# Performance work log

Hardware: AMD Instinct MI355X
Metric: run time of the kernel (lower is better)

Reference implementation:

```python
import jax, jax.numpy as jnp
import numpy as np

B, S, D, N, HD, M = 2, 2048, 1024, 16, 64, 4096  # batch, seq, d_model, heads, head_dim, d_mlp


def setup_inputs() -> dict:
    key = jax.random.key(0)
    ks = jax.random.split(key, 8)
    sd = 1.0 / np.sqrt(D)
    return {
        "x": jax.random.normal(ks[0], (B, S, D), dtype=jnp.float32),
        "W_qkv": jax.random.normal(ks[1], (N, D, 3 * HD), dtype=jnp.float32) * sd,
        "W_out": jax.random.normal(ks[2], (N, HD, D), dtype=jnp.float32) * sd,
        "ln1_w": jnp.ones((D,), jnp.float32),
        "ln1_b": jnp.zeros((D,), jnp.float32),
        "ln2_w": jnp.ones((D,), jnp.float32),
        "ln2_b": jnp.zeros((D,), jnp.float32),
        "W1": jax.random.normal(ks[3], (D, M), dtype=jnp.float32) * sd,
        "b1": jnp.zeros((M,), jnp.float32),
        "W2": jax.random.normal(ks[4], (M, D), dtype=jnp.float32) / np.sqrt(M),
        "b2": jnp.zeros((D,), jnp.float32),
    }


def _layernorm(x, w, b, eps=1e-4):
    mu = jnp.mean(x, axis=-1, keepdims=True)
    var = jnp.var(x, axis=-1, keepdims=True, ddof=1)  # torch unbiased var
    return w * (x - mu) / jnp.sqrt(var + eps) + b


def _attention(x, W_qkv, W_out):
    b, s, d = x.shape
    qkv = jnp.einsum('bsd,ndh->bnsh', x, W_qkv)  # [b,n,s,3*hd]
    q, k, v = jnp.split(qkv, 3, axis=-1)
    hd = q.shape[-1]
    attn = jnp.einsum('bnqh,bnkh->bnqk', q, k) / np.sqrt(hd)
    mask = -1e10 * (1.0 - jnp.tril(jnp.ones((s, s), jnp.float32)))
    attn = jax.nn.softmax(attn + mask, axis=-1)
    out = jnp.einsum('bnqk,bnkh->bnqh', attn, v)  # [b,n,s,hd]
    # faithful to torch: raw memory reinterpretation (b,n,s,hd) -> (b, n*hd, s)
    out = out.reshape(b, -1, s)
    # faithful to torch: d is a shared free index -> W_out summed over (n,h)
    out = jnp.einsum('bds,nhd->bsd', out, W_out)
    return out


def _mlp(x, W1, b1, W2, b2):
    h = jax.nn.gelu(x @ W1 + b1, approximate=False)
    return h @ W2 + b2


def reference(x, W_qkv, W_out, ln1_w, ln1_b, ln2_w, ln2_b, W1, b1, W2, b2):
    x = x + _attention(_layernorm(x, ln1_w, ln1_b), W_qkv, W_out)
    x = x + _mlp(_layernorm(x, ln2_w, ln2_b), W1, b1, W2, b2)
    return x
```

## Files before the change

kernel.cpp:

```cpp
#include <hip/hip_runtime.h>

typedef unsigned short ushort_t;
typedef __attribute__((ext_vector_type(8))) short short8;
typedef __attribute__((ext_vector_type(4))) float floatx4;
typedef __attribute__((ext_vector_type(4))) unsigned short ushort4v;

#define B_ 2
#define S_ 2048
#define D_ 1024
#define NH_ 16
#define HD_ 64
#define M_ 4096

#define KSCALE 0.18033688011112042f

__device__ __forceinline__ ushort_t f2bf(float f) {
    unsigned u = __builtin_bit_cast(unsigned, f);
    return (ushort_t)((u + 0x7FFFu + ((u >> 16) & 1u)) >> 16);
}

__device__ __forceinline__ void gload_lds16(const ushort_t* g, ushort_t* l) {
    __builtin_amdgcn_global_load_lds(
        (const __attribute__((address_space(1))) unsigned int*)(g),
        (__attribute__((address_space(3))) unsigned int*)(l), 16, 0, 0);
}

__device__ __forceinline__ void transpose_slab(
    const float* __restrict__ src, ushort_t* __restrict__ dst,
    int srs, int drs, int by, int bx, int tid, ushort_t* L) {
    const int tx = tid & 15, ty = tid >> 4;
    const float* s0 = src + (size_t)(by * 256 + ty * 4) * srs + bx * 64 + tx * 4;
    #pragma unroll
    for (int i = 0; i < 4; ++i) {
        float a[4][4];
        #pragma unroll
        for (int r = 0; r < 4; ++r) {
            float4 m = *(const float4*)(s0 + (size_t)(i * 64 + r) * srs);
            a[r][0] = m.x; a[r][1] = m.y; a[r][2] = m.z; a[r][3] = m.w;
        }
        const int p = i * 8 + (ty >> 1), plow = ty & 1;
        #pragma unroll
        for (int j = 0; j < 4; ++j) {
            const int c = tx * 4 + j;
            const int pp = p ^ tx;
            ushort4v t;
            t[0] = f2bf(a[0][j]); t[1] = f2bf(a[1][j]);
            t[2] = f2bf(a[2][j]); t[3] = f2bf(a[3][j]);
            *(ushort4v*)&L[c * 256 + (pp * 2 + plow) * 4] = t;
        }
    }
    __syncthreads();
    const int k = tid & 31, cg = tid >> 5;
    #pragma unroll
    for (int it = 0; it < 8; ++it) {
        const int c = it * 8 + cg;
        const int pp = k ^ (c >> 2);
        *(short8*)(dst + (size_t)(bx * 64 + c) * drs + by * 256 + k * 8) =
            *(const short8*)&L[c * 256 + pp * 8];
    }
}

__device__ __forceinline__ void ln_row_wave(const float* __restrict__ x,
                                            const float* __restrict__ w,
                                            const float* __restrict__ b,
                                            ushort_t* __restrict__ out, int row, int l) {
    const float* xr = x + (size_t)row * D_;
    float4 v[4]; float s = 0.f, ss = 0.f;
    #pragma unroll
    for (int i = 0; i < 4; ++i) {
        v[i] = *(const float4*)(xr + (i * 64 + l) * 4);
        s += v[i].x + v[i].y + v[i].z + v[i].w;
        ss += v[i].x * v[i].x + v[i].y * v[i].y + v[i].z * v[i].z + v[i].w * v[i].w;
    }
    #pragma unroll
    for (int off = 32; off >= 1; off >>= 1) { s += __shfl_xor(s, off); ss += __shfl_xor(ss, off); }
    float mu = s * (1.f / D_);
    float var = (ss - (float)D_ * mu * mu) * (1.f / (D_ - 1));
    float rstd = rsqrtf(var + 1e-4f);
    #pragma unroll
    for (int i = 0; i < 4; ++i) {
        int d = (i * 64 + l) * 4;
        float4 wv = *(const float4*)(w + d);
        float4 bv = *(const float4*)(b + d);
        ushort4v o;
        o[0] = f2bf((v[i].x - mu) * rstd * wv.x + bv.x);
        o[1] = f2bf((v[i].y - mu) * rstd * wv.y + bv.y);
        o[2] = f2bf((v[i].z - mu) * rstd * wv.z + bv.z);
        o[3] = f2bf((v[i].w - mu) * rstd * wv.w + bv.w);
        *(ushort4v*)&out[(size_t)row * D_ + d] = o;
    }
}

__global__ __launch_bounds__(256) void ln4_kernel(const float* __restrict__ x,
                                                  const float* __restrict__ w,
                                                  const float* __restrict__ b,
                                                  ushort_t* __restrict__ out) {
    ln_row_wave(x, w, b, out, blockIdx.x * 4 + (threadIdx.x >> 6), threadIdx.x & 63);
}

__global__ __launch_bounds__(256) void prep_kernel(
    const float* __restrict__ W_qkv, const float* __restrict__ W1,
    const float* __restrict__ W2, const float* __restrict__ W_out,
    ushort_t* __restrict__ WqkvT, ushort_t* __restrict__ W1T,
    ushort_t* __restrict__ W2T, float* __restrict__ wsum,
    const float* __restrict__ x, const float* __restrict__ ln1_w,
    const float* __restrict__ ln1_b, ushort_t* __restrict__ ln1_out) {
    __shared__ __align__(16) ushort_t L[64 * 256];
    const int bid = blockIdx.x;
    const int tid = threadIdx.x;
    if (bid < 192) {
        int bz = bid / 12, rem = bid % 12;
        transpose_slab(W_qkv + (size_t)bz * D_ * 192, WqkvT + (size_t)bz * 192 * D_,
                       192, D_, rem / 3, rem % 3, tid, L);
    } else if (bid < 448) {
        int r = bid - 192;
        transpose_slab(W1, W1T, M_, D_, r >> 6, r & 63, tid, L);
    } else if (bid < 704) {
        int r = bid - 448;
        transpose_slab(W2, W2T, D_, M_, r >> 4, r & 15, tid, L);
    } else if (bid < 712) {
        int cb = bid - 704;
        float4* part = (float4*)L;
        int tx = tid & 31, rg = tid >> 5;
        int col = cb * 128 + tx * 4;
        float4 s = {0.f, 0.f, 0.f, 0.f};
        for (int r = rg; r < NH_ * HD_; r += 8) {
            float4 v = *(const float4*)(W_out + (size_t)r * D_ + col);
            s.x += v.x; s.y += v.y; s.z += v.z; s.w += v.w;
        }
        part[tid] = s;
        __syncthreads();
        if (tid < 32) {
            float4 t = {0.f, 0.f, 0.f, 0.f};
            #pragma unroll
            for (int g = 0; g < 8; ++g) {
                float4 p = part[g * 32 + tid];
                t.x += p.x; t.y += p.y; t.z += p.z; t.w += p.w;
            }
            *(float4*)(wsum + cb * 128 + tid * 4) = t;
        }
    } else {
        ln_row_wave(x, ln1_w, ln1_b, ln1_out, (bid - 712) * 4 + (tid >> 6), tid & 63);
    }
}

__global__ __launch_bounds__(256) void gather_resid(
    const float* __restrict__ x, const float* __restrict__ attn,
    const float* __restrict__ wsum, float* __restrict__ x1) {
    __shared__ float tile[128][65];
    const int tid = threadIdx.x;
    const int dchunk = blockIdx.x;
    const int stile = blockIdx.y;
    const int b = stile >> 5, shi = stile & 31;
    const int h = tid & 63;
    const int wv = tid >> 6;
    #pragma unroll
    for (int r = 0; r < 32; ++r) {
        int dloc = r * 4 + wv;
        int d = dchunk * 128 + dloc;
        int q = ((d & 63) << 5) + shi;
        tile[dloc][h] = attn[((size_t)(b * NH_ + (d >> 6)) * S_ + q) * HD_ + h];
    }
    __syncthreads();
    const int row0 = b * S_ + shi * 64;
    const int dcol = tid & 127;
    const int d = dchunk * 128 + dcol;
    const float wsd = wsum[d];
    #pragma unroll
    for (int r = 0; r < 32; ++r) {
        int sr = r * 2 + (tid >> 7);
        size_t idx = (size_t)(row0 + sr) * D_ + d;
        x1[idx] = x[idx] + wsd * tile[dcol][sr];
    }
}

__global__ __launch_bounds__(256) void mlp2_reduce(
    const float* __restrict__ part, const float* __restrict__ x1,
    const float* __restrict__ b2, float* __restrict__ out) {
    int i = blockIdx.x * 256 + threadIdx.x;
    #pragma unroll
    for (int it = 0; it < 4; ++it, i += 1024 * 256) {
        size_t o = (size_t)i * 4;
        float4 s = *(const float4*)(x1 + o);
        float4 bb = *(const float4*)(b2 + ((i * 4) & (D_ - 1)));
        s.x += bb.x; s.y += bb.y; s.z += bb.z; s.w += bb.w;
        #pragma unroll
        for (int z = 0; z < 2; ++z) {
            float4 p = *(const float4*)(part + (size_t)z * ((size_t)B_ * S_ * D_) + o);
            s.x += p.x; s.y += p.y; s.z += p.z; s.w += p.w;
        }
        *(float4*)(out + o) = s;
    }
}

template <int EPI>
__global__ __launch_bounds__(256) void gemm_bt(
    const ushort_t* __restrict__ A, const ushort_t* __restrict__ BT,
    int M, int N, int K, int ld, const float* __restrict__ bias,
    void* __restrict__ outp, void* __restrict__ outp2) {
    __shared__ __align__(16) ushort_t As[128 * 64];
    __shared__ __align__(16) ushort_t Bs[128 * 64];
    const int tid = threadIdx.x;
    const int lane = tid & 63, wave = tid >> 6;
    const int ln15 = lane & 15, qd = lane >> 4;
    const int wm = wave >> 1, wn = wave & 1;
    const int bm = blockIdx.y, bn = blockIdx.x;
    const int lr = lane >> 3;
    const int sw = (lane & 7) ^ lr;
    if (EPI == 4) {
        A += (size_t)blockIdx.z * K;
        BT += (size_t)blockIdx.z * K;
    }

    floatx4 acc[4][4];
    #pragma unroll
    for (int i = 0; i < 4; ++i)
        #pragma unroll
        for (int j = 0; j < 4; ++j) acc[i][j] = (floatx4){0.f, 0.f, 0.f, 0.f};

    for (int k0 = 0; k0 < K; k0 += 64) {
        __syncthreads();
        #pragma unroll
        for (int l = 0; l < 4; ++l) {
            int r0 = (l * 4 + wave) * 8;
            gload_lds16(A + (size_t)(bm * 128 + r0 + lr) * ld + k0 + sw * 8, &As[r0 * 64]);
            gload_lds16(BT + (size_t)(bn * 128 + r0 + lr) * ld + k0 + sw * 8, &Bs[r0 * 64]);
        }
        __syncthreads();
        #pragma unroll
        for (int ks = 0; ks < 2; ++ks) {
            short8 a[4], b[4];
            #pragma unroll
            for (int mt = 0; mt < 4; ++mt) {
                int row = wm * 64 + mt * 16 + ln15;
                a[mt] = *(const short8*)&As[row * 64 + (((ks * 4 + qd) ^ (row & 7)) << 3)];
            }
            #pragma unroll
            for (int nt = 0; nt < 4; ++nt) {
                int row = wn * 64 + nt * 16 + ln15;
                b[nt] = *(const short8*)&Bs[row * 64 + (((ks * 4 + qd) ^ (row & 7)) << 3)];
            }
            #pragma unroll
            for (int mt = 0; mt < 4; ++mt)
                #pragma unroll
                for (int nt = 0; nt < 4; ++nt)
                    acc[mt][nt] = __builtin_amdgcn_mfma_f32_16x16x32_bf16(a[mt], b[nt], acc[mt][nt], 0, 0, 0);
        }
    }

    const int row0 = bm * 128 + wm * 64, col0 = bn * 128 + wn * 64;
    #pragma unroll
    for (int mt = 0; mt < 4; ++mt)
        #pragma unroll
        for (int nt = 0; nt < 4; ++nt) {
            if (EPI == 0) {
                int col = col0 + nt * 16 + ln15;
                unsigned uc = (unsigned)col;
                unsigned hn = uc / 192u;
                unsigned j = uc - hn * 192u;
                int rowb = row0 + mt * 16 + qd * 4;
                int bb = rowb >> 11, sidx = rowb & 2047;
                if (j < 128u) {
                    #pragma unroll
                    for (int r = 0; r < 4; ++r) {
                        float v = acc[mt][nt][r];
                        if (j >= 64u) v *= KSCALE;
                        ((ushort_t*)outp)[(((size_t)bb * NH_ + hn) * S_ + sidx + r) * 192 + j] = f2bf(v);
                    }
                } else {
                    ushort4v pk;
                    #pragma unroll
                    for (int r = 0; r < 4; ++r) pk[r] = f2bf(acc[mt][nt][r]);
                    *(ushort4v*)&((ushort_t*)outp2)[((size_t)(bb * NH_ + hn) * HD_ + (j - 128u)) * S_ + sidx] = pk;
                }
            } else {
                #pragma unroll
                for (int r = 0; r < 4; ++r) {
                    int row = row0 + mt * 16 + qd * 4 + r;
                    int col = col0 + nt * 16 + ln15;
                    float v = acc[mt][nt][r];
                    if (EPI == 1) {
                        v += bias[col];
                        float u = v * (0.7978845608f + 0.0356774081f * v * v);
                        float e = exp2f(fminf(u * 2.88539008f, 80.f));
                        float rc = __builtin_amdgcn_rcpf(e + 1.f);
                        float g = v * (1.f - rc);
                        ((ushort_t*)outp)[(size_t)row * N + col] = f2bf(g);
                    } else {
                        ((float*)outp)[(size_t)blockIdx.z * ((size_t)B_ * S_ * D_) +
                                       (size_t)row * N + col] = v;
                    }
                }
            }
        }
}

__global__ __launch_bounds__(256) void attn_kernel(const ushort_t* __restrict__ qkv,
                                                   const ushort_t* __restrict__ vT,
                                                   float* __restrict__ attn_out) {
    __shared__ __align__(16) ushort_t Ks[128 * 64];
    __shared__ __align__(16) ushort_t Vs[64 * 128];
    __shared__ __align__(16) ushort_t Ps[4][16 * 72];
    const int tid = threadIdx.x, lane = tid & 63, w = tid >> 6;
    const int ln15 = lane & 15, qd = lane >> 4;
    const int px = blockIdx.x;
    const int bh = blockIdx.z * NH_ + blockIdx.y;
    const size_t qbase = (size_t)bh * S_ * 192;
    const size_t vtbase = (size_t)bh * HD_ * S_;
    ushort_t* myP = (ushort_t*)Ps[w];

    #pragma unroll 1
    for (int pq = 0; pq < 2; ++pq) {
        const int qt = pq ? px : 31 - px;
        const int qb = qt * 64 + w * 16;

        const ushort_t* qrow = qkv + qbase + (size_t)(qb + ln15) * 192;
        short8 bq[2];
        bq[0] = *(const short8*)(qrow + qd * 8);
        bq[1] = *(const short8*)(qrow + 32 + qd * 8);

        float lcur = 0.f;
        floatx4 oacc[4];
        #pragma unroll
        for (int mt = 0; mt < 4; ++mt) oacc[mt] = (floatx4){0.f, 0.f, 0.f, 0.f};

        auto qk_half = [&](int kh, floatx4* s) {
            #pragma unroll
            for (int mt = 0; mt < 4; ++mt) s[mt] = (floatx4){0.f, 0.f, 0.f, 0.f};
            #pragma unroll
            for (int ks = 0; ks < 2; ++ks)
                #pragma unroll
                for (int mt = 0; mt < 4; ++mt) {
                    int row = kh * 64 + mt * 16 + ln15;
                    short8 ak = *(const short8*)&Ks[row * 64 + (((ks * 4 + qd) ^ (row & 7)) << 3)];
                    s[mt] = __builtin_amdgcn_mfma_f32_16x16x32_bf16(ak, bq[ks], s[mt], 0, 0, 0);
                }
        };
        auto softmax_pv = [&](floatx4* s, int kh, bool mask) {
            if (mask) {
                int q = qb + ln15;
                #pragma unroll
                for (int mt = 0; mt < 4; ++mt)
                    #pragma unroll
                    for (int r = 0; r < 4; ++r)
                        if (qt * 64 + mt * 16 + qd * 4 + r > q) s[mt][r] = -1e30f;
            }
            float rsum = 0.f;
            #pragma unroll
            for (int mt = 0; mt < 4; ++mt) {
                ushort4v pk;
                #pragma unroll
                for (int r = 0; r < 4; ++r) {
                    float p = exp2f(s[mt][r]);
                    rsum += p;
                    pk[r] = (ushort_t)(__builtin_bit_cast(unsigned, p) >> 16);
                }
                *(ushort4v*)&myP[ln15 * 72 + mt * 16 + qd * 4] = pk;
            }
            rsum += __shfl_xor(rsum, 16);
            rsum += __shfl_xor(rsum, 32);
            lcur += rsum;
            #pragma unroll
            for (int g2 = 0; g2 < 2; ++g2) {
                short8 bp = *(const short8*)&myP[ln15 * 72 + g2 * 32 + qd * 8];
                #pragma unroll
                for (int mt = 0; mt < 4; ++mt) {
                    int row = mt * 16 + ln15;
                    short8 av = *(const short8*)&Vs[row * 128 + (((kh * 8 + g2 * 4 + qd) ^ (row & 15)) << 3)];
                    oacc[mt] = __builtin_amdgcn_mfma_f32_16x16x32_bf16(av, bp, oacc[mt], 0, 0, 0);
                }
            }
        };

        const int ntiles = qt + 1;
        for (int kt2 = 0; kt2 < ntiles; kt2 += 2) {
            __syncthreads();
            #pragma unroll
            for (int i = 0; i < 4; ++i) {
                int gb = (i * 4 + w) * 64;
                int g = gb + lane;
                int krow = g >> 3;
                int kcg = (g & 7) ^ (krow & 7);
                int key = kt2 * 64 + krow; if (key > S_ - 1) key = S_ - 1;
                gload_lds16(qkv + qbase + (size_t)key * 192 + 64 + kcg * 8, &Ks[gb * 8]);
                int vrow = g >> 4;
                int vcg = (g & 15) ^ (vrow & 15);
                int vkey = kt2 * 64 + vcg * 8; if (vkey > S_ - 8) vkey = S_ - 8;
                gload_lds16(vT + vtbase + (size_t)vrow * S_ + vkey, &Vs[gb * 8]);
            }
            __syncthreads();

            if (kt2 + 1 < ntiles) {
                floatx4 s0[4], s1[4];
                qk_half(0, s0);
                qk_half(1, s1);
                softmax_pv(s0, 0, false);
                softmax_pv(s1, 1, kt2 + 1 == qt);
            } else {
                floatx4 s0[4];
                qk_half(0, s0);
                softmax_pv(s0, 0, kt2 == qt);
            }
        }
        float inv = 1.f / lcur;
        int q = qb + ln15;
        #pragma unroll
        for (int mt = 0; mt < 4; ++mt) {
            floatx4 o = oacc[mt] * inv;
            *(floatx4*)&attn_out[((size_t)bh * S_ + q) * HD_ + mt * 16 + qd * 4] = o;
        }
    }
}

extern "C" void kernel_launch(void* const* d_in, const int* in_sizes, int n_in,
                              void* d_out, int out_size, void* d_ws, size_t ws_size,
                              hipStream_t stream) {
    const float* x = (const float*)d_in[0];
    const float* W_qkv = (const float*)d_in[1];
    const float* W_out = (const float*)d_in[2];
    const float* ln1_w = (const float*)d_in[3];
    const float* ln1_b = (const float*)d_in[4];
    const float* ln2_w = (const float*)d_in[5];
    const float* ln2_b = (const float*)d_in[6];
    const float* W1 = (const float*)d_in[7];
    const float* b1 = (const float*)d_in[8];
    const float* W2 = (const float*)d_in[9];
    const float* b2 = (const float*)d_in[10];

    char* ws = (char*)d_ws;
    const size_t MB = 1024 * 1024;
    ushort_t* ln1_out = (ushort_t*)(ws + 0 * MB);
    ushort_t* WqkvT   = (ushort_t*)(ws + 8 * MB);
    ushort_t* qkv     = (ushort_t*)(ws + 14 * MB);
    ushort_t* vT      = (ushort_t*)(ws + 38 * MB);
    float*    attn_o  = (float*)(ws + 46 * MB);
    float*    x1      = (float*)(ws + 64 * MB);
    ushort_t* ln2_out = (ushort_t*)(ws + 80 * MB);
    ushort_t* W1T     = (ushort_t*)(ws + 88 * MB);
    ushort_t* hbuf    = (ushort_t*)(ws + 96 * MB);
    ushort_t* W2T     = (ushort_t*)(ws + 128 * MB);
    float*    wsum    = (float*)(ws + 136 * MB);
    float*    mlp2p   = (float*)(ws + 0 * MB);

    prep_kernel<<<dim3(712 + 1024), 256, 0, stream>>>(
        W_qkv, W1, W2, W_out, WqkvT, W1T, W2T, wsum, x, ln1_w, ln1_b, ln1_out);
    gemm_bt<0><<<dim3(3072 / 128, (B_ * S_) / 128), 256, 0, stream>>>(
        ln1_out, WqkvT, B_ * S_, 3072, D_, D_, nullptr, qkv, vT);
    attn_kernel<<<dim3(S_ / 128, NH_, B_), 256, 0, stream>>>(qkv, vT, attn_o);
    gather_resid<<<dim3(8, 64), 256, 0, stream>>>(x, attn_o, wsum, x1);
    ln4_kernel<<<dim3(1024), 256, 0, stream>>>(x1, ln2_w, ln2_b, ln2_out);
    gemm_bt<1><<<dim3(M_ / 128, (B_ * S_) / 128), 256, 0, stream>>>(
        ln2_out, W1T, B_ * S_, M_, D_, D_, b1, hbuf, nullptr);
    gemm_bt<4><<<dim3(D_ / 128, (B_ * S_) / 128, 2), 256, 0, stream>>>(
        hbuf, W2T, B_ * S_, D_, M_ / 2, M_, nullptr, mlp2p, nullptr);
    mlp2_reduce<<<dim3(1024), 256, 0, stream>>>(mlp2p, x1, b2, (float*)d_out);
}
```

Measured before the change: 388.1 us.

## Double-buffer GEMM LDS tiles with split-K halves and vmcnt-based pipelining

Rewrites the bf16 GEMM main loop to use two LDS slots, each split into two 32-wide K halves. The next tile's halves are prefetched via global_load_lds while the current slot is computed, with s_waitcnt vmcnt plus raw barriers replacing the double __syncthreads. The LDS swizzle is changed to fit the 32-element rows, and MFMA blocks are bracketed with s_setprio. This aims to hide global-load latency behind MFMA work, at the cost of doubling LDS use to 64KB per block, which may reduce occupancy.

```diff
diff --git a/kernel.cpp b/kernel.cpp
--- a/kernel.cpp
+++ b/kernel.cpp
@@ -198,19 +198,36 @@
     const ushort_t* __restrict__ A, const ushort_t* __restrict__ BT,
     int M, int N, int K, int ld, const float* __restrict__ bias,
     void* __restrict__ outp, void* __restrict__ outp2) {
-    __shared__ __align__(16) ushort_t As[128 * 64];
-    __shared__ __align__(16) ushort_t Bs[128 * 64];
+    __shared__ __align__(16) ushort_t As[16384];
+    __shared__ __align__(16) ushort_t Bs[16384];
     const int tid = threadIdx.x;
-    const int lane = tid & 63, wave = tid >> 6;
+    const int lane = tid & 63;
     const int ln15 = lane & 15, qd = lane >> 4;
+    const int wave = tid >> 6;
     const int wm = wave >> 1, wn = wave & 1;
     const int bm = blockIdx.y, bn = blockIdx.x;
-    const int lr = lane >> 3;
-    const int sw = (lane & 7) ^ lr;
     if (EPI == 4) {
         A += (size_t)blockIdx.z * K;
         BT += (size_t)blockIdx.z * K;
     }
+    const int rA = tid >> 2;
+    const int g8 = (((tid & 3) ^ ((rA >> 1) & 3)) << 3);
+    const ushort_t* Ab = A + (size_t)(bm * 128 + rA) * ld + g8;
+    const ushort_t* Bb = BT + (size_t)(bn * 128 + rA) * ld + g8;
+    const size_t rstep = (size_t)64 * ld;
+    ushort_t* Ad = As + tid * 8;
+    ushort_t* Bd = Bs + tid * 8;
+
+    auto stage = [&](int slot, int h, int kc) {
+        const ushort_t* as = Ab + kc + h * 32;
+        const ushort_t* bs = Bb + kc + h * 32;
+        ushort_t* ad = Ad + slot * 8192 + h * 4096;
+        ushort_t* bd = Bd + slot * 8192 + h * 4096;
+        gload_lds16(as, ad);
+        gload_lds16(as + rstep, ad + 2048);
+        gload_lds16(bs, bd);
+        gload_lds16(bs + rstep, bd + 2048);
+    };
 
     floatx4 acc[4][4];
     #pragma unroll
@@ -218,43 +235,66 @@
         #pragma unroll
         for (int j = 0; j < 4; ++j) acc[i][j] = (floatx4){0.f, 0.f, 0.f, 0.f};
 
-    for (int k0 = 0; k0 < K; k0 += 64) {
-        __syncthreads();
-        #pragma unroll
-        for (int l = 0; l < 4; ++l) {
-            int r0 = (l * 4 + wave) * 8;
-            gload_lds16(A + (size_t)(bm * 128 + r0 + lr) * ld + k0 + sw * 8, &As[r0 * 64]);
-            gload_lds16(BT + (size_t)(bn * 128 + r0 + lr) * ld + k0 + sw * 8, &Bs[r0 * 64]);
-        }
-        __syncthreads();
-        #pragma unroll
-        for (int ks = 0; ks < 2; ++ks) {
-            short8 a[4], b[4];
-            #pragma unroll
-            for (int mt = 0; mt < 4; ++mt) {
-                int row = wm * 64 + mt * 16 + ln15;
-                a[mt] = *(const short8*)&As[row * 64 + (((ks * 4 + qd) ^ (row & 7)) << 3)];
-            }
-            #pragma unroll
-            for (int nt = 0; nt < 4; ++nt) {
-                int row = wn * 64 + nt * 16 + ln15;
-                b[nt] = *(const short8*)&Bs[row * 64 + (((ks * 4 + qd) ^ (row & 7)) << 3)];
-            }
-            #pragma unroll
-            for (int mt = 0; mt < 4; ++mt)
-                #pragma unroll
-                for (int nt = 0; nt < 4; ++nt)
-                    acc[mt][nt] = __builtin_amdgcn_mfma_f32_16x16x32_bf16(a[mt], b[nt], acc[mt][nt], 0, 0, 0);
-        }
+    auto compute = [&](int slot, int ks) {
+        short8 a[4], b[4];
+        const ushort_t* ap = As + slot * 8192 + ks * 4096;
+        const ushort_t* bp = Bs + slot * 8192 + ks * 4096;
+        #pragma unroll
+        for (int mt = 0; mt < 4; ++mt) {
+            int row = wm * 64 + mt * 16 + ln15;
+            a[mt] = *(const short8*)&ap[row * 32 + ((qd ^ ((row >> 1) & 3)) << 3)];
+        }
+        #pragma unroll
+        for (int nt = 0; nt < 4; ++nt) {
+            int row = wn * 64 + nt * 16 + ln15;
+            b[nt] = *(const short8*)&bp[row * 32 + ((qd ^ ((row >> 1) & 3)) << 3)];
+        }
+        __builtin_amdgcn_s_setprio(1);
+        #pragma unroll
+        for (int mt = 0; mt < 4; ++mt)
+            #pragma unroll
+            for (int nt = 0; nt < 4; ++nt)
+                acc[mt][nt] = __builtin_amdgcn_mfma_f32_16x16x32_bf16(a[mt], b[nt], acc[mt][nt], 0, 0, 0);
+        __builtin_amdgcn_s_setprio(0);
+    };
+
+    const int nt = K >> 6;
+    stage(0, 0, 0);
+    stage(0, 1, 0);
+    #pragma unroll 1
+    for (int t = 0; t < nt - 1; ++t) {
+        const int slot = t & 1, nslot = slot ^ 1;
+        const int kn = (t + 1) << 6;
+        stage(nslot, 0, kn);
+        asm volatile("s_waitcnt vmcnt(8)" ::: "memory");
+        __builtin_amdgcn_s_barrier();
+        __builtin_amdgcn_sched_barrier(0);
+        compute(slot, 0);
+        stage(nslot, 1, kn);
+        asm volatile("s_waitcnt vmcnt(8)" ::: "memory");
+        __builtin_amdgcn_s_barrier();
+        __builtin_amdgcn_sched_barrier(0);
+        compute(slot, 1);
+    }
+    {
+        const int slot = (nt - 1) & 1;
+        asm volatile("s_waitcnt vmcnt(4)" ::: "memory");
+        __builtin_amdgcn_s_barrier();
+        __builtin_amdgcn_sched_barrier(0);
+        compute(slot, 0);
+        asm volatile("s_waitcnt vmcnt(0)" ::: "memory");
+        __builtin_amdgcn_s_barrier();
+        __builtin_amdgcn_sched_barrier(0);
+        compute(slot, 1);
     }
 
     const int row0 = bm * 128 + wm * 64, col0 = bn * 128 + wn * 64;
     #pragma unroll
     for (int mt = 0; mt < 4; ++mt)
         #pragma unroll
-        for (int nt = 0; nt < 4; ++nt) {
+        for (int nt2 = 0; nt2 < 4; ++nt2) {
             if (EPI == 0) {
-                int col = col0 + nt * 16 + ln15;
+                int col = col0 + nt2 * 16 + ln15;
                 unsigned uc = (unsigned)col;
                 unsigned hn = uc / 192u;
                 unsigned j = uc - hn * 192u;
@@ -263,22 +303,22 @@
                 if (j < 128u) {
                     #pragma unroll
                     for (int r = 0; r < 4; ++r) {
-                        float v = acc[mt][nt][r];
+                        float v = acc[mt][nt2][r];
                         if (j >= 64u) v *= KSCALE;
                         ((ushort_t*)outp)[(((size_t)bb * NH_ + hn) * S_ + sidx + r) * 192 + j] = f2bf(v);
                     }
                 } else {
                     ushort4v pk;
                     #pragma unroll
-                    for (int r = 0; r < 4; ++r) pk[r] = f2bf(acc[mt][nt][r]);
+                    for (int r = 0; r < 4; ++r) pk[r] = f2bf(acc[mt][nt2][r]);
                     *(ushort4v*)&((ushort_t*)outp2)[((size_t)(bb * NH_ + hn) * HD_ + (j - 128u)) * S_ + sidx] = pk;
                 }
             } else {
                 #pragma unroll
                 for (int r = 0; r < 4; ++r) {
                     int row = row0 + mt * 16 + qd * 4 + r;
-                    int col = col0 + nt * 16 + ln15;
-                    float v = acc[mt][nt][r];
+                    int col = col0 + nt2 * 16 + ln15;
+                    float v = acc[mt][nt2][r];
                     if (EPI == 1) {
                         v += bias[col];
                         float u = v * (0.7978845608f + 0.0356774081f * v * v);
```

Measured after the change: 393.3 us. No clear change (+1.3%).

## Replace 128x128 GEMM with 256x256 four-stage pipelined kernel and split-K 4

Applied to the files above, without the earlier changes.

The GEMM kernel grows from 128x128 to 256x256 tiles, with 512 threads per block and 8x4 MFMA accumulators per wave. A 4-deep LDS ring is filled by direct global-to-LDS loads, using explicit vmcnt waits, raw barriers and setprio around the MFMA bursts, so loads overlap compute. The second MLP GEMM now splits K four ways instead of two, and the reduce kernel sums four partials. The goal is more data reuse per tile, less barrier and load latency stall, and enough blocks to fill the CUs. The cost is 128KB of LDS per block, so only one block fits per CU. The split-K partial buffer also grows to fill exactly the workspace region below x1.

```diff
diff --git a/kernel.cpp b/kernel.cpp
--- a/kernel.cpp
+++ b/kernel.cpp
@@ -23,6 +23,13 @@
     __builtin_amdgcn_global_load_lds(
         (const __attribute__((address_space(1))) unsigned int*)(g),
         (__attribute__((address_space(3))) unsigned int*)(l), 16, 0, 0);
+}
+
+__device__ __forceinline__ void waitv(int n) {
+    if (n >= 12)      asm volatile("s_waitcnt vmcnt(12)" ::: "memory");
+    else if (n == 8)  asm volatile("s_waitcnt vmcnt(8)" ::: "memory");
+    else if (n == 4)  asm volatile("s_waitcnt vmcnt(4)" ::: "memory");
+    else              asm volatile("s_waitcnt vmcnt(0)" ::: "memory");
 }
 
 __device__ __forceinline__ void transpose_slab(
@@ -185,7 +192,7 @@
         float4 bb = *(const float4*)(b2 + ((i * 4) & (D_ - 1)));
         s.x += bb.x; s.y += bb.y; s.z += bb.z; s.w += bb.w;
         #pragma unroll
-        for (int z = 0; z < 2; ++z) {
+        for (int z = 0; z < 4; ++z) {
             float4 p = *(const float4*)(part + (size_t)z * ((size_t)B_ * S_ * D_) + o);
             s.x += p.x; s.y += p.y; s.z += p.z; s.w += p.w;
         }
@@ -194,91 +201,125 @@
 }
 
 template <int EPI>
-__global__ __launch_bounds__(256) void gemm_bt(
+__global__ __launch_bounds__(512, 2) void gemm256(
     const ushort_t* __restrict__ A, const ushort_t* __restrict__ BT,
     int M, int N, int K, int ld, const float* __restrict__ bias,
     void* __restrict__ outp, void* __restrict__ outp2) {
-    __shared__ __align__(16) ushort_t As[128 * 64];
-    __shared__ __align__(16) ushort_t Bs[128 * 64];
+    __shared__ __align__(16) ushort_t Abuf[4 * 8192];
+    __shared__ __align__(16) ushort_t Bbuf[4 * 8192];
     const int tid = threadIdx.x;
-    const int lane = tid & 63, wave = tid >> 6;
+    const int lane = tid & 63;
     const int ln15 = lane & 15, qd = lane >> 4;
-    const int wm = wave >> 1, wn = wave & 1;
+    const int wave = tid >> 6;
+    const int wm = wave >> 2, wn = wave & 3;
     const int bm = blockIdx.y, bn = blockIdx.x;
-    const int lr = lane >> 3;
-    const int sw = (lane & 7) ^ lr;
     if (EPI == 4) {
         A += (size_t)blockIdx.z * K;
         BT += (size_t)blockIdx.z * K;
     }
 
-    floatx4 acc[4][4];
-    #pragma unroll
-    for (int i = 0; i < 4; ++i)
+    const int gi0 = tid, gi1 = 512 + tid;
+    const int rp0 = gi0 >> 3, x0 = (gi0 & 7) ^ (rp0 & 7);
+    const int rp1 = gi1 >> 3, x1 = (gi1 & 7) ^ (rp1 & 7);
+    const int r0 = rp0 * 2 + (x0 >> 2), g0 = x0 & 3;
+    const int r1 = rp1 * 2 + (x1 >> 2), g1 = x1 & 3;
+    const ushort_t* As0 = A + (size_t)(bm * 256 + r0) * ld + g0 * 8;
+    const ushort_t* As1 = A + (size_t)(bm * 256 + r1) * ld + g1 * 8;
+    const ushort_t* Bs0 = BT + (size_t)(bn * 256 + r0) * ld + g0 * 8;
+    const ushort_t* Bs1 = BT + (size_t)(bn * 256 + r1) * ld + g1 * 8;
+    ushort_t* Ad0 = Abuf + gi0 * 8;  ushort_t* Ad1 = Abuf + gi1 * 8;
+    ushort_t* Bd0 = Bbuf + gi0 * 8;  ushort_t* Bd1 = Bbuf + gi1 * 8;
+
+    auto stage = [&](int sp) {
+        const int koff = (sp >> 2) * 128 + (sp & 3) * 32;
+        const int boff = (sp & 3) * 8192;
+        gload_lds16(As0 + koff, Ad0 + boff);
+        gload_lds16(As1 + koff, Ad1 + boff);
+        gload_lds16(Bs0 + koff, Bd0 + boff);
+        gload_lds16(Bs1 + koff, Bd1 + boff);
+    };
+
+    floatx4 acc[8][4];
+    #pragma unroll
+    for (int i = 0; i < 8; ++i)
         #pragma unroll
         for (int j = 0; j < 4; ++j) acc[i][j] = (floatx4){0.f, 0.f, 0.f, 0.f};
 
-    for (int k0 = 0; k0 < K; k0 += 64) {
-        __syncthreads();
-        #pragma unroll
-        for (int l = 0; l < 4; ++l) {
-            int r0 = (l * 4 + wave) * 8;
-            gload_lds16(A + (size_t)(bm * 128 + r0 + lr) * ld + k0 + sw * 8, &As[r0 * 64]);
-            gload_lds16(BT + (size_t)(bn * 128 + r0 + lr) * ld + k0 + sw * 8, &Bs[r0 * 64]);
-        }
-        __syncthreads();
-        #pragma unroll
-        for (int ks = 0; ks < 2; ++ks) {
-            short8 a[4], b[4];
-            #pragma unroll
-            for (int mt = 0; mt < 4; ++mt) {
-                int row = wm * 64 + mt * 16 + ln15;
-                a[mt] = *(const short8*)&As[row * 64 + (((ks * 4 + qd) ^ (row & 7)) << 3)];
-            }
-            #pragma unroll
-            for (int nt = 0; nt < 4; ++nt) {
-                int row = wn * 64 + nt * 16 + ln15;
-                b[nt] = *(const short8*)&Bs[row * 64 + (((ks * 4 + qd) ^ (row & 7)) << 3)];
-            }
-            #pragma unroll
-            for (int mt = 0; mt < 4; ++mt)
-                #pragma unroll
-                for (int nt = 0; nt < 4; ++nt)
-                    acc[mt][nt] = __builtin_amdgcn_mfma_f32_16x16x32_bf16(a[mt], b[nt], acc[mt][nt], 0, 0, 0);
-        }
-    }
-
-    const int row0 = bm * 128 + wm * 64, col0 = bn * 128 + wn * 64;
-    #pragma unroll
-    for (int mt = 0; mt < 4; ++mt)
-        #pragma unroll
-        for (int nt = 0; nt < 4; ++nt) {
+    auto frag = [&](const ushort_t* buf, int row) -> short8 {
+        int rp = row >> 1;
+        int pos = (((row & 1) << 2) | qd) ^ (rp & 7);
+        return *(const short8*)&buf[rp * 64 + pos * 8];
+    };
+
+    auto compute = [&](int sb) {
+        const ushort_t* ap = Abuf + sb * 8192;
+        const ushort_t* bp = Bbuf + sb * 8192;
+        short8 a[8], b[4];
+        #pragma unroll
+        for (int m = 0; m < 8; ++m) a[m] = frag(ap, wm * 128 + m * 16 + ln15);
+        #pragma unroll
+        for (int n = 0; n < 4; ++n) b[n] = frag(bp, wn * 64 + n * 16 + ln15);
+        __builtin_amdgcn_s_setprio(1);
+        #pragma unroll
+        for (int m = 0; m < 8; ++m)
+            #pragma unroll
+            for (int n = 0; n < 4; ++n)
+                acc[m][n] = __builtin_amdgcn_mfma_f32_16x16x32_bf16(a[m], b[n], acc[m][n], 0, 0, 0);
+        __builtin_amdgcn_s_setprio(0);
+    };
+
+    const int NT = K >> 7;
+    const int last = 4 * NT - 1;
+    stage(0); stage(1); stage(2);
+    #pragma unroll 1
+    for (int t = 0; t < NT; ++t) {
+        #pragma unroll
+        for (int q = 0; q < 4; ++q) {
+            const int ph = t * 4 + q;
+            const int sp = ph + 3;
+            if (sp <= last) stage(sp);
+            const int rem = last - ph;
+            waitv(rem >= 3 ? 12 : rem * 4);
+            __builtin_amdgcn_s_barrier();
+            __builtin_amdgcn_sched_barrier(0);
+            compute(q);
+            __builtin_amdgcn_sched_barrier(0);
+            __builtin_amdgcn_s_barrier();
+            __builtin_amdgcn_sched_barrier(0);
+        }
+    }
+
+    const int row0 = bm * 256 + wm * 128, col0 = bn * 256 + wn * 64;
+    #pragma unroll
+    for (int m = 0; m < 8; ++m)
+        #pragma unroll
+        for (int n = 0; n < 4; ++n) {
             if (EPI == 0) {
-                int col = col0 + nt * 16 + ln15;
+                int col = col0 + n * 16 + ln15;
                 unsigned uc = (unsigned)col;
                 unsigned hn = uc / 192u;
                 unsigned j = uc - hn * 192u;
-                int rowb = row0 + mt * 16 + qd * 4;
+                int rowb = row0 + m * 16 + qd * 4;
                 int bb = rowb >> 11, sidx = rowb & 2047;
                 if (j < 128u) {
                     #pragma unroll
                     for (int r = 0; r < 4; ++r) {
-                        float v = acc[mt][nt][r];
+                        float v = acc[m][n][r];
                         if (j >= 64u) v *= KSCALE;
                         ((ushort_t*)outp)[(((size_t)bb * NH_ + hn) * S_ + sidx + r) * 192 + j] = f2bf(v);
                     }
                 } else {
                     ushort4v pk;
                     #pragma unroll
-                    for (int r = 0; r < 4; ++r) pk[r] = f2bf(acc[mt][nt][r]);
+                    for (int r = 0; r < 4; ++r) pk[r] = f2bf(acc[m][n][r]);
                     *(ushort4v*)&((ushort_t*)outp2)[((size_t)(bb * NH_ + hn) * HD_ + (j - 128u)) * S_ + sidx] = pk;
                 }
             } else {
                 #pragma unroll
                 for (int r = 0; r < 4; ++r) {
-                    int row = row0 + mt * 16 + qd * 4 + r;
-                    int col = col0 + nt * 16 + ln15;
-                    float v = acc[mt][nt][r];
+                    int row = row0 + m * 16 + qd * 4 + r;
+                    int col = col0 + n * 16 + ln15;
+                    float v = acc[m][n][r];
                     if (EPI == 1) {
                         v += bias[col];
                         float u = v * (0.7978845608f + 0.0356774081f * v * v);
@@ -444,14 +485,14 @@
 
     prep_kernel<<<dim3(712 + 1024), 256, 0, stream>>>(
         W_qkv, W1, W2, W_out, WqkvT, W1T, W2T, wsum, x, ln1_w, ln1_b, ln1_out);
-    gemm_bt<0><<<dim3(3072 / 128, (B_ * S_) / 128), 256, 0, stream>>>(
+    gemm256<0><<<dim3(3072 / 256, (B_ * S_) / 256), 512, 0, stream>>>(
         ln1_out, WqkvT, B_ * S_, 3072, D_, D_, nullptr, qkv, vT);
     attn_kernel<<<dim3(S_ / 128, NH_, B_), 256, 0, stream>>>(qkv, vT, attn_o);
     gather_resid<<<dim3(8, 64), 256, 0, stream>>>(x, attn_o, wsum, x1);
     ln4_kernel<<<dim3(1024), 256, 0, stream>>>(x1, ln2_w, ln2_b, ln2_out);
-    gemm_bt<1><<<dim3(M_ / 128, (B_ * S_) / 128), 256, 0, stream>>>(
+    gemm256<1><<<dim3(M_ / 256, (B_ * S_) / 256), 512, 0, stream>>>(
         ln2_out, W1T, B_ * S_, M_, D_, D_, b1, hbuf, nullptr);
-    gemm_bt<4><<<dim3(D_ / 128, (B_ * S_) / 128, 2), 256, 0, stream>>>(
-        hbuf, W2T, B_ * S_, D_, M_ / 2, M_, nullptr, mlp2p, nullptr);
+    gemm256<4><<<dim3(D_ / 256, (B_ * S_) / 256, 4), 512, 0, stream>>>(
+        hbuf, W2T, B_ * S_, D_, M_ / 4, M_, nullptr, mlp2p, nullptr);
     mlp2_reduce<<<dim3(1024), 256, 0, stream>>>(mlp2p, x1, b2, (float*)d_out);
 }
```

Result: no change. 382.9 us (-1.3%).
